# Optimization experiments

Hardware: AMD Instinct MI355X
Metric: run time of the kernel (lower is better)

Reference implementation:

```python
import jax, jax.numpy as jnp
import numpy as np

D_MODEL = 1024
DK = 64
N_HEADS = D_MODEL // DK
MASK = True


def setup_inputs() -> dict:
    key = jax.random.key(0)
    ks = jax.random.split(key, 8)
    B, S = 4, 2048
    scale = 1.0 / np.sqrt(D_MODEL)
    return {
        "query_data": jax.random.normal(ks[0], (B, S, D_MODEL), dtype=jnp.float32),
        "key_data": jax.random.normal(ks[1], (B, S, D_MODEL), dtype=jnp.float32),
        "value_data": jax.random.normal(ks[2], (B, S, D_MODEL), dtype=jnp.float32),
        "Wq": jax.random.normal(ks[3], (D_MODEL, D_MODEL), dtype=jnp.float32) * scale,
        "Wk": jax.random.normal(ks[4], (D_MODEL, D_MODEL), dtype=jnp.float32) * scale,
        "Wv": jax.random.normal(ks[5], (D_MODEL, D_MODEL), dtype=jnp.float32) * scale,
        "Wp": jax.random.normal(ks[6], (D_MODEL, D_MODEL), dtype=jnp.float32) * scale,
        "bp": jnp.zeros((D_MODEL,), dtype=jnp.float32),
    }


def reference(query_data, key_data, value_data, Wq, Wk, Wv, Wp, bp):
    B, S, _ = query_data.shape
    # QKV projections, split into heads: (B, H, S, dk)
    def split_heads(x, W):
        return (x @ W.T).reshape(B, -1, N_HEADS, DK).transpose(0, 2, 1, 3)

    q = split_heads(query_data, Wq)
    k = split_heads(key_data, Wk)
    v = split_heads(value_data, Wv)

    scores = jnp.einsum("bhqd,bhkd->bhqk", q, k) / np.sqrt(DK).astype(np.float32)
    if MASK:
        Sq, Sk = scores.shape[-2], scores.shape[-1]
        causal = jnp.triu(jnp.ones((Sq, Sk), dtype=scores.dtype), k=1) * jnp.float32(-1e13)
        scores = scores + causal  # broadcast over (B, H)
    attn = jax.nn.softmax(scores, axis=-1)
    out = jnp.einsum("bhqk,bhkd->bhqd", attn, v)
    out = out.transpose(0, 2, 1, 3).reshape(B, S, D_MODEL)
    # dropout is identity in eval mode
    return out @ Wp.T + bp
```

## Files before the change

### kernel.cpp

```cpp
#include <hip/hip_runtime.h>
#include <stdint.h>

#define D_MODEL 1024
#define SEQ     2048
#define BATCH   4
#define NH      16
#define DKK     64
#define MROWS   (BATCH * SEQ)

typedef unsigned short u16;
using bf16x8 = __attribute__((ext_vector_type(8))) __bf16;
using f32x4  = __attribute__((ext_vector_type(4))) float;

__device__ __forceinline__ u16 f2bf(float f) {
    union { float f; uint32_t u; } v; v.f = f;
    return (u16)((v.u + 0x7FFFu + ((v.u >> 16) & 1u)) >> 16);
}

__device__ __forceinline__ float fast_exp2(float x) {
    float r; asm("v_exp_f32 %0, %1" : "=v"(r) : "v"(x)); return r;
}
__device__ __forceinline__ float fast_rcp(float x) {
    float r; asm("v_rcp_f32 %0, %1" : "=v"(r) : "v"(x)); return r;
}

__device__ __forceinline__ void gl_lds16(const u16* g, u16* l) {
    __builtin_amdgcn_global_load_lds(
        (__attribute__((address_space(1))) void*)(const_cast<u16*>(g)),
        (__attribute__((address_space(3))) void*)l, 16, 0, 0);
}

__global__ __launch_bounds__(256) void cvt3_kernel(const float* __restrict__ a,
                                                   const float* __restrict__ b,
                                                   const float* __restrict__ c,
                                                   u16* __restrict__ da,
                                                   u16* __restrict__ db,
                                                   u16* __restrict__ dc) {
    const int i = blockIdx.x * 256 + threadIdx.x;
    const int sel = i >> 21, off = i & ((1 << 21) - 1);
    const float* s = (sel == 0) ? a : (sel == 1) ? b : c;
    u16* d = (sel == 0) ? da : (sel == 1) ? db : dc;
    float4 v = ((const float4*)s)[off];
    ushort4 o;
    o.x = f2bf(v.x); o.y = f2bf(v.y); o.z = f2bf(v.z); o.w = f2bf(v.w);
    ((ushort4*)d)[off] = o;
}

__global__ __launch_bounds__(256) void cvt4_kernel(const float* __restrict__ a,
                                                   const float* __restrict__ b,
                                                   const float* __restrict__ c,
                                                   const float* __restrict__ d4,
                                                   u16* __restrict__ da,
                                                   u16* __restrict__ db,
                                                   u16* __restrict__ dc,
                                                   u16* __restrict__ dd) {
    const int i = blockIdx.x * 256 + threadIdx.x;
    const int sel = i >> 18, off = i & ((1 << 18) - 1);
    const float* s = (sel == 0) ? a : (sel == 1) ? b : (sel == 2) ? c : d4;
    u16* d = (sel == 0) ? da : (sel == 1) ? db : (sel == 2) ? dc : dd;
    float4 v = ((const float4*)s)[off];
    ushort4 o;
    o.x = f2bf(v.x); o.y = f2bf(v.y); o.z = f2bf(v.z); o.w = f2bf(v.w);
    ((ushort4*)d)[off] = o;
}

__global__ __launch_bounds__(256, 2) void gemm_qkv(const u16* __restrict__ XQ,
                                                   const u16* __restrict__ XK,
                                                   const u16* __restrict__ XV,
                                                   const u16* __restrict__ WQ,
                                                   const u16* __restrict__ WK,
                                                   const u16* __restrict__ WV,
                                                   u16* __restrict__ Qo,
                                                   u16* __restrict__ Ko,
                                                   u16* __restrict__ Vto) {
    constexpr int K = 1024, N = 1024;
    __shared__ __align__(16) u16 smem[17408];
    u16* ldsA = smem;
    u16* ldsB = smem + 4096;
    u16* ldsT = smem;

    const int which = blockIdx.x >> 9;
    const int inner = blockIdx.x & 511;
    const u16* A  = (which == 0) ? XQ : (which == 1) ? XK : XV;
    const u16* Bw = (which == 0) ? WQ : (which == 1) ? WK : WV;

    const int t = threadIdx.x;
    const int w = t >> 6, lane = t & 63;
    const int quad = lane >> 4, l15 = lane & 15;
    const int bn = inner & 7, bm = inner >> 3;
    const int wm = (w >> 1) * 64, wn = (w & 1) * 64;

    const u16* Ab = A  + (size_t)bm * 128 * K;
    const u16* Bb = Bw + (size_t)bn * 128 * K;
    const int srow  = lane >> 2;
    const int scol8 = (lane & 3) * 8;

    f32x4 acc[4][4];
    #pragma unroll
    for (int i = 0; i < 4; ++i)
        #pragma unroll
        for (int j = 0; j < 4; ++j)
            acc[i][j] = f32x4{0.f, 0.f, 0.f, 0.f};

    for (int k0 = 0; k0 < K; k0 += 32) {
        __syncthreads();
        #pragma unroll
        for (int i = 0; i < 2; ++i) {
            const int c = w * 2 + i;
            gl_lds16(Ab + (size_t)(c * 16 + srow) * K + k0 + scol8, &ldsA[c * 512]);
            gl_lds16(Bb + (size_t)(c * 16 + srow) * K + k0 + scol8, &ldsB[c * 512]);
        }
        __syncthreads();

        bf16x8 afr[4], bfr[4];
        #pragma unroll
        for (int i = 0; i < 4; ++i)
            afr[i] = *(const bf16x8*)&ldsA[(wm + i * 16 + l15) * 32 + quad * 8];
        #pragma unroll
        for (int j = 0; j < 4; ++j)
            bfr[j] = *(const bf16x8*)&ldsB[(wn + j * 16 + l15) * 32 + quad * 8];

        #pragma unroll
        for (int i = 0; i < 4; ++i)
            #pragma unroll
            for (int j = 0; j < 4; ++j)
                acc[i][j] = __builtin_amdgcn_mfma_f32_16x16x32_bf16(afr[i], bfr[j], acc[i][j], 0, 0, 0);
    }

    if (which < 2) {
        u16* outb = which ? Ko : Qo;
        #pragma unroll
        for (int i = 0; i < 4; ++i)
            #pragma unroll
            for (int j = 0; j < 4; ++j)
                #pragma unroll
                for (int r = 0; r < 4; ++r) {
                    const int row = bm * 128 + wm + i * 16 + quad * 4 + r;
                    const int col = bn * 128 + wn + j * 16 + l15;
                    outb[(size_t)row * N + col] = f2bf(acc[i][j][r]);
                }
    } else {
        __syncthreads();
        #pragma unroll
        for (int i = 0; i < 4; ++i)
            #pragma unroll
            for (int j = 0; j < 4; ++j)
                #pragma unroll
                for (int r = 0; r < 4; ++r) {
                    const int row_l = wm + i * 16 + quad * 4 + r;
                    const int col_l = wn + j * 16 + l15;
                    ldsT[col_l * 136 + row_l] = f2bf(acc[i][j][r]);
                }
        __syncthreads();
        const int c = t >> 1, half = t & 1;
        const int colg = bn * 128 + c;
        const int hh = colg >> 6, dd = colg & 63;
        const int bb = bm >> 4;
        const int s0 = ((bm * 128) & 2047) + half * 64;
        const u16* srcl = ldsT + c * 136 + half * 64;
        u16* dstg = Vto + (size_t)((bb * NH + hh) * DKK + dd) * SEQ + s0;
        #pragma unroll
        for (int k = 0; k < 8; ++k)
            *(uint4*)(dstg + k * 8) = *(const uint4*)(srcl + k * 8);
    }
}

__global__ __launch_bounds__(256, 2) void gemm_proj(const u16* __restrict__ A,
                                                    const u16* __restrict__ Bw,
                                                    float* __restrict__ outf,
                                                    const float* __restrict__ bias) {
    constexpr int K = 1024, N = 1024;
    __shared__ __align__(16) u16 ldsA[128 * 32];
    __shared__ __align__(16) u16 ldsB[128 * 32];

    const int t = threadIdx.x;
    const int w = t >> 6, lane = t & 63;
    const int quad = lane >> 4, l15 = lane & 15;
    const int bn = blockIdx.x & 7, bm = blockIdx.x >> 3;
    const int wm = (w >> 1) * 64, wn = (w & 1) * 64;

    const u16* Ab = A  + (size_t)bm * 128 * K;
    const u16* Bb = Bw + (size_t)bn * 128 * K;
    const int srow  = lane >> 2;
    const int scol8 = (lane & 3) * 8;

    f32x4 acc[4][4];
    #pragma unroll
    for (int i = 0; i < 4; ++i)
        #pragma unroll
        for (int j = 0; j < 4; ++j)
            acc[i][j] = f32x4{0.f, 0.f, 0.f, 0.f};

    for (int k0 = 0; k0 < K; k0 += 32) {
        __syncthreads();
        #pragma unroll
        for (int i = 0; i < 2; ++i) {
            const int c = w * 2 + i;
            gl_lds16(Ab + (size_t)(c * 16 + srow) * K + k0 + scol8, &ldsA[c * 512]);
            gl_lds16(Bb + (size_t)(c * 16 + srow) * K + k0 + scol8, &ldsB[c * 512]);
        }
        __syncthreads();

        bf16x8 afr[4], bfr[4];
        #pragma unroll
        for (int i = 0; i < 4; ++i)
            afr[i] = *(const bf16x8*)&ldsA[(wm + i * 16 + l15) * 32 + quad * 8];
        #pragma unroll
        for (int j = 0; j < 4; ++j)
            bfr[j] = *(const bf16x8*)&ldsB[(wn + j * 16 + l15) * 32 + quad * 8];

        #pragma unroll
        for (int i = 0; i < 4; ++i)
            #pragma unroll
            for (int j = 0; j < 4; ++j)
                acc[i][j] = __builtin_amdgcn_mfma_f32_16x16x32_bf16(afr[i], bfr[j], acc[i][j], 0, 0, 0);
    }

    #pragma unroll
    for (int i = 0; i < 4; ++i)
        #pragma unroll
        for (int j = 0; j < 4; ++j)
            #pragma unroll
            for (int r = 0; r < 4; ++r) {
                const int row = bm * 128 + wm + i * 16 + quad * 4 + r;
                const int col = bn * 128 + wn + j * 16 + l15;
                outf[(size_t)row * N + col] = acc[i][j][r] + bias[col];
            }
}

__global__ __launch_bounds__(256, 4) void flash_attn(const u16* __restrict__ Qb,
                                                     const u16* __restrict__ Kb,
                                                     const u16* __restrict__ Vt,
                                                     u16* __restrict__ O) {
    __shared__ __align__(16) u16 ldsK[2 * 4096];
    __shared__ __align__(16) u16 ldsV[2 * 4096];
    __shared__ __align__(16) u16 ldsP[4 * 1024];

    const int t = threadIdx.x;
    const int w = t >> 6, lane = t & 63;
    const int quad = lane >> 4, l15 = lane & 15;
    const int bh = blockIdx.x & 63;
    const int qt = 31 - (blockIdx.x >> 6);
    const int b = bh >> 4, h = bh & 15;
    const int q0 = qt * 64;
    const int qw = q0 + w * 16;

    const int srow  = lane >> 2;
    const int scol8 = (lane & 3) * 8;
    const size_t kbase = (size_t)b * SEQ * D_MODEL + h * DKK;
    const size_t vbase = (size_t)(bh * DKK) * SEQ;

    const u16* Qrow = Qb + (size_t)(b * SEQ + qw + l15) * D_MODEL + h * DKK;
    const bf16x8 qf0 = *(const bf16x8*)(Qrow + quad * 8);
    const bf16x8 qf1 = *(const bf16x8*)(Qrow + 32 + quad * 8);

    f32x4 o_acc[4];
    #pragma unroll
    for (int nt = 0; nt < 4; ++nt) o_acc[nt] = f32x4{0.f, 0.f, 0.f, 0.f};
    float m_i = -1e30f, l_i = 0.f;

    const float C2 = 0.18033688f;

    u16* PwS = &ldsP[w * 1024 + l15 * 64];

    {
        #pragma unroll
        for (int i = 0; i < 2; ++i) {
            const int e = w * 2 + i, ch = e >> 2, rb = (e & 3) * 16;
            gl_lds16(Kb + kbase + (size_t)(rb + srow) * D_MODEL + ch * 32 + scol8,
                     &ldsK[ch * 2048 + rb * 32]);
            gl_lds16(Vt + vbase + (size_t)(rb + srow) * SEQ + ch * 32 + scol8,
                     &ldsV[ch * 2048 + rb * 32]);
        }
    }

    int cur = 0;
    for (int it = 0; it <= qt; ++it) {
        const int kb = it * 64;
        __syncthreads();

        if (it < qt) {
            const int nb = (it + 1) * 64, nxt = cur ^ 1;
            #pragma unroll
            for (int i = 0; i < 2; ++i) {
                const int e = w * 2 + i, ch = e >> 2, rb = (e & 3) * 16;
                gl_lds16(Kb + kbase + (size_t)(nb + rb + srow) * D_MODEL + ch * 32 + scol8,
                         &ldsK[nxt * 4096 + ch * 2048 + rb * 32]);
                gl_lds16(Vt + vbase + (size_t)(rb + srow) * SEQ + nb + ch * 32 + scol8,
                         &ldsV[nxt * 4096 + ch * 2048 + rb * 32]);
            }
        }

        f32x4 sc[4];
        #pragma unroll
        for (int jt = 0; jt < 4; ++jt) sc[jt] = f32x4{0.f, 0.f, 0.f, 0.f};
        #pragma unroll
        for (int ks = 0; ks < 2; ++ks) {
            const bf16x8 qf = ks ? qf1 : qf0;
            #pragma unroll
            for (int jt = 0; jt < 4; ++jt) {
                bf16x8 kf = *(const bf16x8*)&ldsK[cur * 4096 + ks * 2048 + (jt * 16 + l15) * 32 + quad * 8];
                sc[jt] = __builtin_amdgcn_mfma_f32_16x16x32_bf16(kf, qf, sc[jt], 0, 0, 0);
            }
        }

        if (kb + 63 > qw) {
            #pragma unroll
            for (int jt = 0; jt < 4; ++jt)
                #pragma unroll
                for (int r = 0; r < 4; ++r)
                    if (kb + jt * 16 + quad * 4 + r > qw + l15) sc[jt][r] = -3.0e38f;
        }

        float tmax = sc[0][0];
        #pragma unroll
        for (int jt = 0; jt < 4; ++jt)
            #pragma unroll
            for (int r = 0; r < 4; ++r) tmax = fmaxf(tmax, sc[jt][r]);
        tmax = fmaxf(tmax, __shfl_xor(tmax, 16));
        tmax = fmaxf(tmax, __shfl_xor(tmax, 32));

        const float mn = fmaxf(m_i, tmax * C2);
        const float alpha = fast_exp2(m_i - mn);
        m_i = mn;

        float tsum = 0.f;
        #pragma unroll
        for (int jt = 0; jt < 4; ++jt) {
            float p[4];
            #pragma unroll
            for (int r = 0; r < 4; ++r) {
                p[r] = fast_exp2(fmaf(sc[jt][r], C2, -mn));
                tsum += p[r];
            }
            const int pos = (4 * jt + quad) ^ l15;
            uint2 pk;
            pk.x = (uint32_t)f2bf(p[0]) | ((uint32_t)f2bf(p[1]) << 16);
            pk.y = (uint32_t)f2bf(p[2]) | ((uint32_t)f2bf(p[3]) << 16);
            *(uint2*)&PwS[pos * 4] = pk;
        }
        tsum += __shfl_xor(tsum, 16);
        tsum += __shfl_xor(tsum, 32);
        l_i = fmaf(l_i, alpha, tsum);

        float al[4];
        #pragma unroll
        for (int r = 0; r < 4; ++r)
            al[r] = __shfl(alpha, (lane & 48) | (quad * 4 + r));
        #pragma unroll
        for (int nt = 0; nt < 4; ++nt)
            #pragma unroll
            for (int r = 0; r < 4; ++r)
                o_acc[nt][r] *= al[r];

        asm volatile("s_waitcnt lgkmcnt(0)" ::: "memory");

        #pragma unroll
        for (int ks = 0; ks < 2; ++ks) {
            const int g = 8 * ks + 2 * quad;
            uint2 lo = *(const uint2*)&PwS[((g    ) ^ l15) * 4];
            uint2 hi = *(const uint2*)&PwS[((g + 1) ^ l15) * 4];
            union { bf16x8 v; uint2 u[2]; } pu;
            pu.u[0] = lo; pu.u[1] = hi;
            #pragma unroll
            for (int nt = 0; nt < 4; ++nt) {
                bf16x8 vf = *(const bf16x8*)&ldsV[cur * 4096 + ks * 2048 + (nt * 16 + l15) * 32 + quad * 8];
                o_acc[nt] = __builtin_amdgcn_mfma_f32_16x16x32_bf16(pu.v, vf, o_acc[nt], 0, 0, 0);
            }
        }

        cur ^= 1;
    }

    const float rli = fast_rcp(l_i);
    float rl[4];
    #pragma unroll
    for (int r = 0; r < 4; ++r)
        rl[r] = __shfl(rli, (lane & 48) | (quad * 4 + r));
    #pragma unroll
    for (int nt = 0; nt < 4; ++nt)
        #pragma unroll
        for (int r = 0; r < 4; ++r) {
            const int qg = qw + quad * 4 + r;
            O[(size_t)(b * SEQ + qg) * D_MODEL + h * DKK + nt * 16 + l15] = f2bf(o_acc[nt][r] * rl[r]);
        }
}

extern "C" void kernel_launch(void* const* d_in, const int* in_sizes, int n_in,
                              void* d_out, int out_size, void* d_ws, size_t ws_size,
                              hipStream_t stream) {
    const float* q_in = (const float*)d_in[0];
    const float* k_in = (const float*)d_in[1];
    const float* v_in = (const float*)d_in[2];
    const float* Wq   = (const float*)d_in[3];
    const float* Wk   = (const float*)d_in[4];
    const float* Wv   = (const float*)d_in[5];
    const float* Wp   = (const float*)d_in[6];
    const float* bp   = (const float*)d_in[7];
    float* out = (float*)d_out;

    char* ws = (char*)d_ws;
    u16* XQ  = (u16*)(ws + (size_t)0);
    u16* XK  = (u16*)(ws + ((size_t)16 << 20));
    u16* XV  = (u16*)(ws + ((size_t)32 << 20));
    u16* WQb = (u16*)(ws + ((size_t)48 << 20));
    u16* WKb = (u16*)(ws + ((size_t)50 << 20));
    u16* WVb = (u16*)(ws + ((size_t)52 << 20));
    u16* WPb = (u16*)(ws + ((size_t)54 << 20));
    u16* Qb  = (u16*)(ws + ((size_t)56 << 20));
    u16* Kb  = (u16*)(ws + ((size_t)72 << 20));
    u16* Vtb = (u16*)(ws + ((size_t)88 << 20));

    cvt3_kernel<<<3 * (1 << 21) / 256, 256, 0, stream>>>(q_in, k_in, v_in, XQ, XK, XV);
    cvt4_kernel<<<4 * (1 << 18) / 256, 256, 0, stream>>>(Wq, Wk, Wv, Wp, WQb, WKb, WVb, WPb);

    gemm_qkv<<<1536, 256, 0, stream>>>(XQ, XK, XV, WQb, WKb, WVb, Qb, Kb, Vtb);

    flash_attn<<<BATCH * NH * (SEQ / 64), 256, 0, stream>>>(Qb, Kb, Vtb, XQ);

    gemm_proj<<<512, 256, 0, stream>>>(XQ, WPb, out, bp);
}
```

Measured before the change: 347.8 us.

## Double-buffer GEMMs, swizzle tiles, and widen attention to 128-row query tiles

Both projection GEMMs now prefetch the next K slice into a second LDS buffer, drop one barrier per step, and remap blocks so neighbours share input tiles in L2. Flash attention now handles 128 queries per block with two 16-row groups per wave, reusing each K and V fragment twice and skipping key tiles that are fully masked for a wave. The fp32 to bf16 conversions use the packed rounding intrinsic, and launch bounds are retuned. The changes cost more registers and LDS per block and so may reduce occupancy, and they introduce per-wave load imbalance in attention.

Result: faster. 305.6 us (-12.1%).

```diff
diff --git a/kernel.cpp b/kernel.cpp
--- a/kernel.cpp
+++ b/kernel.cpp
@@ -1,4 +1,5 @@
 #include <hip/hip_runtime.h>
+#include <hip/hip_bf16.h>
 #include <stdint.h>
 
 #define D_MODEL 1024
@@ -15,6 +16,11 @@
 __device__ __forceinline__ u16 f2bf(float f) {
     union { float f; uint32_t u; } v; v.f = f;
     return (u16)((v.u + 0x7FFFu + ((v.u >> 16) & 1u)) >> 16);
+}
+__device__ __forceinline__ uint32_t pk2bf(float a, float b) {
+    union { __hip_bfloat162 h; uint32_t u; } v;
+    v.h = __float22bfloat162_rn(float2{a, b});
+    return v.u;
 }
 
 __device__ __forceinline__ float fast_exp2(float x) {
@@ -41,9 +47,9 @@
     const float* s = (sel == 0) ? a : (sel == 1) ? b : c;
     u16* d = (sel == 0) ? da : (sel == 1) ? db : dc;
     float4 v = ((const float4*)s)[off];
-    ushort4 o;
-    o.x = f2bf(v.x); o.y = f2bf(v.y); o.z = f2bf(v.z); o.w = f2bf(v.w);
-    ((ushort4*)d)[off] = o;
+    uint2 o;
+    o.x = pk2bf(v.x, v.y); o.y = pk2bf(v.z, v.w);
+    ((uint2*)d)[off] = o;
 }
 
 __global__ __launch_bounds__(256) void cvt4_kernel(const float* __restrict__ a,
@@ -59,12 +65,12 @@
     const float* s = (sel == 0) ? a : (sel == 1) ? b : (sel == 2) ? c : d4;
     u16* d = (sel == 0) ? da : (sel == 1) ? db : (sel == 2) ? dc : dd;
     float4 v = ((const float4*)s)[off];
-    ushort4 o;
-    o.x = f2bf(v.x); o.y = f2bf(v.y); o.z = f2bf(v.z); o.w = f2bf(v.w);
-    ((ushort4*)d)[off] = o;
-}
-
-__global__ __launch_bounds__(256, 2) void gemm_qkv(const u16* __restrict__ XQ,
+    uint2 o;
+    o.x = pk2bf(v.x, v.y); o.y = pk2bf(v.z, v.w);
+    ((uint2*)d)[off] = o;
+}
+
+__global__ __launch_bounds__(256, 3) void gemm_qkv(const u16* __restrict__ XQ,
                                                    const u16* __restrict__ XK,
                                                    const u16* __restrict__ XV,
                                                    const u16* __restrict__ WQ,
@@ -76,7 +82,7 @@
     constexpr int K = 1024, N = 1024;
     __shared__ __align__(16) u16 smem[17408];
     u16* ldsA = smem;
-    u16* ldsB = smem + 4096;
+    u16* ldsB = smem + 8192;
     u16* ldsT = smem;
 
     const int which = blockIdx.x >> 9;
@@ -87,7 +93,8 @@
     const int t = threadIdx.x;
     const int w = t >> 6, lane = t & 63;
     const int quad = lane >> 4, l15 = lane & 15;
-    const int bn = inner & 7, bm = inner >> 3;
+    const int x = inner & 7, j = inner >> 3;
+    const int bm = x * 8 + (j >> 3), bn = j & 7;
     const int wm = (w >> 1) * 64, wn = (w & 1) * 64;
 
     const u16* Ab = A  + (size_t)bm * 128 * K;
@@ -99,32 +106,43 @@
     #pragma unroll
     for (int i = 0; i < 4; ++i)
         #pragma unroll
-        for (int j = 0; j < 4; ++j)
-            acc[i][j] = f32x4{0.f, 0.f, 0.f, 0.f};
-
+        for (int jj = 0; jj < 4; ++jj)
+            acc[i][jj] = f32x4{0.f, 0.f, 0.f, 0.f};
+
+    #pragma unroll
+    for (int i = 0; i < 2; ++i) {
+        const int c = w * 2 + i;
+        gl_lds16(Ab + (size_t)(c * 16 + srow) * K + scol8, &ldsA[c * 512]);
+        gl_lds16(Bb + (size_t)(c * 16 + srow) * K + scol8, &ldsB[c * 512]);
+    }
+
+    int cur = 0;
     for (int k0 = 0; k0 < K; k0 += 32) {
         __syncthreads();
-        #pragma unroll
-        for (int i = 0; i < 2; ++i) {
-            const int c = w * 2 + i;
-            gl_lds16(Ab + (size_t)(c * 16 + srow) * K + k0 + scol8, &ldsA[c * 512]);
-            gl_lds16(Bb + (size_t)(c * 16 + srow) * K + k0 + scol8, &ldsB[c * 512]);
+        if (k0 + 32 < K) {
+            const int nxt = cur ^ 1;
+            #pragma unroll
+            for (int i = 0; i < 2; ++i) {
+                const int c = w * 2 + i;
+                gl_lds16(Ab + (size_t)(c * 16 + srow) * K + k0 + 32 + scol8, &ldsA[nxt * 4096 + c * 512]);
+                gl_lds16(Bb + (size_t)(c * 16 + srow) * K + k0 + 32 + scol8, &ldsB[nxt * 4096 + c * 512]);
+            }
         }
-        __syncthreads();
 
         bf16x8 afr[4], bfr[4];
         #pragma unroll
         for (int i = 0; i < 4; ++i)
-            afr[i] = *(const bf16x8*)&ldsA[(wm + i * 16 + l15) * 32 + quad * 8];
-        #pragma unroll
-        for (int j = 0; j < 4; ++j)
-            bfr[j] = *(const bf16x8*)&ldsB[(wn + j * 16 + l15) * 32 + quad * 8];
-
-        #pragma unroll
-        for (int i = 0; i < 4; ++i)
-            #pragma unroll
-            for (int j = 0; j < 4; ++j)
-                acc[i][j] = __builtin_amdgcn_mfma_f32_16x16x32_bf16(afr[i], bfr[j], acc[i][j], 0, 0, 0);
+            afr[i] = *(const bf16x8*)&ldsA[cur * 4096 + (wm + i * 16 + l15) * 32 + quad * 8];
+        #pragma unroll
+        for (int jj = 0; jj < 4; ++jj)
+            bfr[jj] = *(const bf16x8*)&ldsB[cur * 4096 + (wn + jj * 16 + l15) * 32 + quad * 8];
+
+        #pragma unroll
+        for (int i = 0; i < 4; ++i)
+            #pragma unroll
+            for (int jj = 0; jj < 4; ++jj)
+                acc[i][jj] = __builtin_amdgcn_mfma_f32_16x16x32_bf16(afr[i], bfr[jj], acc[i][jj], 0, 0, 0);
+        cur ^= 1;
     }
 
     if (which < 2) {
@@ -132,24 +150,24 @@
         #pragma unroll
         for (int i = 0; i < 4; ++i)
             #pragma unroll
-            for (int j = 0; j < 4; ++j)
+            for (int jj = 0; jj < 4; ++jj)
                 #pragma unroll
                 for (int r = 0; r < 4; ++r) {
                     const int row = bm * 128 + wm + i * 16 + quad * 4 + r;
-                    const int col = bn * 128 + wn + j * 16 + l15;
-                    outb[(size_t)row * N + col] = f2bf(acc[i][j][r]);
+                    const int col = bn * 128 + wn + jj * 16 + l15;
+                    outb[(size_t)row * N + col] = f2bf(acc[i][jj][r]);
                 }
     } else {
         __syncthreads();
         #pragma unroll
         for (int i = 0; i < 4; ++i)
             #pragma unroll
-            for (int j = 0; j < 4; ++j)
+            for (int jj = 0; jj < 4; ++jj)
                 #pragma unroll
                 for (int r = 0; r < 4; ++r) {
                     const int row_l = wm + i * 16 + quad * 4 + r;
-                    const int col_l = wn + j * 16 + l15;
-                    ldsT[col_l * 136 + row_l] = f2bf(acc[i][j][r]);
+                    const int col_l = wn + jj * 16 + l15;
+                    ldsT[col_l * 136 + row_l] = f2bf(acc[i][jj][r]);
                 }
         __syncthreads();
         const int c = t >> 1, half = t & 1;
@@ -165,18 +183,19 @@
     }
 }
 
-__global__ __launch_bounds__(256, 2) void gemm_proj(const u16* __restrict__ A,
+__global__ __launch_bounds__(256, 3) void gemm_proj(const u16* __restrict__ A,
                                                     const u16* __restrict__ Bw,
                                                     float* __restrict__ outf,
                                                     const float* __restrict__ bias) {
     constexpr int K = 1024, N = 1024;
-    __shared__ __align__(16) u16 ldsA[128 * 32];
-    __shared__ __align__(16) u16 ldsB[128 * 32];
+    __shared__ __align__(16) u16 ldsA[2 * 4096];
+    __shared__ __align__(16) u16 ldsB[2 * 4096];
 
     const int t = threadIdx.x;
     const int w = t >> 6, lane = t & 63;
     const int quad = lane >> 4, l15 = lane & 15;
-    const int bn = blockIdx.x & 7, bm = blockIdx.x >> 3;
+    const int x = blockIdx.x & 7, j = blockIdx.x >> 3;
+    const int bm = x * 8 + ((j & 63) >> 3), bn = j & 7;
     const int wm = (w >> 1) * 64, wn = (w & 1) * 64;
 
     const u16* Ab = A  + (size_t)bm * 128 * K;
@@ -188,99 +207,115 @@
     #pragma unroll
     for (int i = 0; i < 4; ++i)
         #pragma unroll
-        for (int j = 0; j < 4; ++j)
-            acc[i][j] = f32x4{0.f, 0.f, 0.f, 0.f};
-
+        for (int jj = 0; jj < 4; ++jj)
+            acc[i][jj] = f32x4{0.f, 0.f, 0.f, 0.f};
+
+    #pragma unroll
+    for (int i = 0; i < 2; ++i) {
+        const int c = w * 2 + i;
+        gl_lds16(Ab + (size_t)(c * 16 + srow) * K + scol8, &ldsA[c * 512]);
+        gl_lds16(Bb + (size_t)(c * 16 + srow) * K + scol8, &ldsB[c * 512]);
+    }
+
+    int cur = 0;
     for (int k0 = 0; k0 < K; k0 += 32) {
         __syncthreads();
-        #pragma unroll
-        for (int i = 0; i < 2; ++i) {
-            const int c = w * 2 + i;
-            gl_lds16(Ab + (size_t)(c * 16 + srow) * K + k0 + scol8, &ldsA[c * 512]);
-            gl_lds16(Bb + (size_t)(c * 16 + srow) * K + k0 + scol8, &ldsB[c * 512]);
+        if (k0 + 32 < K) {
+            const int nxt = cur ^ 1;
+            #pragma unroll
+            for (int i = 0; i < 2; ++i) {
+                const int c = w * 2 + i;
+                gl_lds16(Ab + (size_t)(c * 16 + srow) * K + k0 + 32 + scol8, &ldsA[nxt * 4096 + c * 512]);
+                gl_lds16(Bb + (size_t)(c * 16 + srow) * K + k0 + 32 + scol8, &ldsB[nxt * 4096 + c * 512]);
+            }
         }
-        __syncthreads();
 
         bf16x8 afr[4], bfr[4];
         #pragma unroll
         for (int i = 0; i < 4; ++i)
-            afr[i] = *(const bf16x8*)&ldsA[(wm + i * 16 + l15) * 32 + quad * 8];
-        #pragma unroll
-        for (int j = 0; j < 4; ++j)
-            bfr[j] = *(const bf16x8*)&ldsB[(wn + j * 16 + l15) * 32 + quad * 8];
-
-        #pragma unroll
-        for (int i = 0; i < 4; ++i)
-            #pragma unroll
-            for (int j = 0; j < 4; ++j)
-                acc[i][j] = __builtin_amdgcn_mfma_f32_16x16x32_bf16(afr[i], bfr[j], acc[i][j], 0, 0, 0);
+            afr[i] = *(const bf16x8*)&ldsA[cur * 4096 + (wm + i * 16 + l15) * 32 + quad * 8];
+        #pragma unroll
+        for (int jj = 0; jj < 4; ++jj)
+            bfr[jj] = *(const bf16x8*)&ldsB[cur * 4096 + (wn + jj * 16 + l15) * 32 + quad * 8];
+
+        #pragma unroll
+        for (int i = 0; i < 4; ++i)
+            #pragma unroll
+            for (int jj = 0; jj < 4; ++jj)
+                acc[i][jj] = __builtin_amdgcn_mfma_f32_16x16x32_bf16(afr[i], bfr[jj], acc[i][jj], 0, 0, 0);
+        cur ^= 1;
     }
 
     #pragma unroll
     for (int i = 0; i < 4; ++i)
         #pragma unroll
-        for (int j = 0; j < 4; ++j)
+        for (int jj = 0; jj < 4; ++jj)
             #pragma unroll
             for (int r = 0; r < 4; ++r) {
                 const int row = bm * 128 + wm + i * 16 + quad * 4 + r;
-                const int col = bn * 128 + wn + j * 16 + l15;
-                outf[(size_t)row * N + col] = acc[i][j][r] + bias[col];
-            }
-}
-
-__global__ __launch_bounds__(256, 4) void flash_attn(const u16* __restrict__ Qb,
+                const int col = bn * 128 + wn + jj * 16 + l15;
+                outf[(size_t)row * N + col] = acc[i][jj][r] + bias[col];
+            }
+}
+
+__global__ __launch_bounds__(256, 3) void flash_attn(const u16* __restrict__ Qb,
                                                      const u16* __restrict__ Kb,
                                                      const u16* __restrict__ Vt,
                                                      u16* __restrict__ O) {
     __shared__ __align__(16) u16 ldsK[2 * 4096];
     __shared__ __align__(16) u16 ldsV[2 * 4096];
-    __shared__ __align__(16) u16 ldsP[4 * 1024];
+    __shared__ __align__(16) u16 ldsP[4 * 2048];
 
     const int t = threadIdx.x;
     const int w = t >> 6, lane = t & 63;
     const int quad = lane >> 4, l15 = lane & 15;
     const int bh = blockIdx.x & 63;
-    const int qt = 31 - (blockIdx.x >> 6);
+    const int qt = 15 - (blockIdx.x >> 6);
     const int b = bh >> 4, h = bh & 15;
-    const int q0 = qt * 64;
-    const int qw = q0 + w * 16;
+    const int q0 = qt * 128;
+    const int qw = q0 + w * 32;
 
     const int srow  = lane >> 2;
     const int scol8 = (lane & 3) * 8;
     const size_t kbase = (size_t)b * SEQ * D_MODEL + h * DKK;
     const size_t vbase = (size_t)(bh * DKK) * SEQ;
 
-    const u16* Qrow = Qb + (size_t)(b * SEQ + qw + l15) * D_MODEL + h * DKK;
-    const bf16x8 qf0 = *(const bf16x8*)(Qrow + quad * 8);
-    const bf16x8 qf1 = *(const bf16x8*)(Qrow + 32 + quad * 8);
-
-    f32x4 o_acc[4];
-    #pragma unroll
-    for (int nt = 0; nt < 4; ++nt) o_acc[nt] = f32x4{0.f, 0.f, 0.f, 0.f};
-    float m_i = -1e30f, l_i = 0.f;
+    bf16x8 qf[2][2];
+    #pragma unroll
+    for (int g = 0; g < 2; ++g) {
+        const u16* Qrow = Qb + (size_t)(b * SEQ + qw + g * 16 + l15) * D_MODEL + h * DKK;
+        qf[g][0] = *(const bf16x8*)(Qrow + quad * 8);
+        qf[g][1] = *(const bf16x8*)(Qrow + 32 + quad * 8);
+    }
+
+    f32x4 o_acc[2][4];
+    #pragma unroll
+    for (int g = 0; g < 2; ++g)
+        #pragma unroll
+        for (int nt = 0; nt < 4; ++nt) o_acc[g][nt] = f32x4{0.f, 0.f, 0.f, 0.f};
+    float m_i[2] = {-1e30f, -1e30f}, l_i[2] = {0.f, 0.f};
 
     const float C2 = 0.18033688f;
-
-    u16* PwS = &ldsP[w * 1024 + l15 * 64];
-
-    {
-        #pragma unroll
-        for (int i = 0; i < 2; ++i) {
-            const int e = w * 2 + i, ch = e >> 2, rb = (e & 3) * 16;
-            gl_lds16(Kb + kbase + (size_t)(rb + srow) * D_MODEL + ch * 32 + scol8,
-                     &ldsK[ch * 2048 + rb * 32]);
-            gl_lds16(Vt + vbase + (size_t)(rb + srow) * SEQ + ch * 32 + scol8,
-                     &ldsV[ch * 2048 + rb * 32]);
-        }
+    u16* PwS = &ldsP[w * 2048];
+
+    const int ntiles = 2 * qt + 2;
+
+    #pragma unroll
+    for (int i = 0; i < 2; ++i) {
+        const int e = w * 2 + i, ch = e >> 2, rb = (e & 3) * 16;
+        gl_lds16(Kb + kbase + (size_t)(rb + srow) * D_MODEL + ch * 32 + scol8,
+                 &ldsK[ch * 2048 + rb * 32]);
+        gl_lds16(Vt + vbase + (size_t)(rb + srow) * SEQ + ch * 32 + scol8,
+                 &ldsV[ch * 2048 + rb * 32]);
     }
 
     int cur = 0;
-    for (int it = 0; it <= qt; ++it) {
+    for (int it = 0; it < ntiles; ++it) {
         const int kb = it * 64;
         __syncthreads();
 
-        if (it < qt) {
-            const int nb = (it + 1) * 64, nxt = cur ^ 1;
+        if (it + 1 < ntiles) {
+            const int nb = kb + 64, nxt = cur ^ 1;
             #pragma unroll
             for (int i = 0; i < 2; ++i) {
                 const int e = w * 2 + i, ch = e >> 2, rb = (e & 3) * 16;
@@ -291,99 +326,119 @@
             }
         }
 
-        f32x4 sc[4];
-        #pragma unroll
-        for (int jt = 0; jt < 4; ++jt) sc[jt] = f32x4{0.f, 0.f, 0.f, 0.f};
-        #pragma unroll
-        for (int ks = 0; ks < 2; ++ks) {
-            const bf16x8 qf = ks ? qf1 : qf0;
-            #pragma unroll
-            for (int jt = 0; jt < 4; ++jt) {
-                bf16x8 kf = *(const bf16x8*)&ldsK[cur * 4096 + ks * 2048 + (jt * 16 + l15) * 32 + quad * 8];
-                sc[jt] = __builtin_amdgcn_mfma_f32_16x16x32_bf16(kf, qf, sc[jt], 0, 0, 0);
+        if (kb <= qw + 31) {
+            f32x4 sc[2][4];
+            #pragma unroll
+            for (int g = 0; g < 2; ++g)
+                #pragma unroll
+                for (int jt = 0; jt < 4; ++jt) sc[g][jt] = f32x4{0.f, 0.f, 0.f, 0.f};
+            #pragma unroll
+            for (int ks = 0; ks < 2; ++ks)
+                #pragma unroll
+                for (int jt = 0; jt < 4; ++jt) {
+                    bf16x8 kf = *(const bf16x8*)&ldsK[cur * 4096 + ks * 2048 + (jt * 16 + l15) * 32 + quad * 8];
+                    #pragma unroll
+                    for (int g = 0; g < 2; ++g)
+                        sc[g][jt] = __builtin_amdgcn_mfma_f32_16x16x32_bf16(kf, qf[g][ks], sc[g][jt], 0, 0, 0);
+                }
+
+            if (kb + 63 >= qw) {
+                #pragma unroll
+                for (int g = 0; g < 2; ++g)
+                    #pragma unroll
+                    for (int jt = 0; jt < 4; ++jt)
+                        #pragma unroll
+                        for (int r = 0; r < 4; ++r)
+                            if (kb + jt * 16 + quad * 4 + r > qw + g * 16 + l15) sc[g][jt][r] = -3.0e38f;
+            }
+
+            float alpha[2];
+            #pragma unroll
+            for (int g = 0; g < 2; ++g) {
+                float tmax = sc[g][0][0];
+                #pragma unroll
+                for (int jt = 0; jt < 4; ++jt)
+                    #pragma unroll
+                    for (int r = 0; r < 4; ++r) tmax = fmaxf(tmax, sc[g][jt][r]);
+                tmax = fmaxf(tmax, __shfl_xor(tmax, 16));
+                tmax = fmaxf(tmax, __shfl_xor(tmax, 32));
+
+                const float mn = fmaxf(m_i[g], tmax * C2);
+                alpha[g] = fast_exp2(m_i[g] - mn);
+                m_i[g] = mn;
+
+                float tsum = 0.f;
+                #pragma unroll
+                for (int jt = 0; jt < 4; ++jt) {
+                    float p[4];
+                    #pragma unroll
+                    for (int r = 0; r < 4; ++r) {
+                        p[r] = fast_exp2(fmaf(sc[g][jt][r], C2, -mn));
+                        tsum += p[r];
+                    }
+                    const int pos = (4 * jt + quad) ^ l15;
+                    uint2 pk;
+                    pk.x = pk2bf(p[0], p[1]);
+                    pk.y = pk2bf(p[2], p[3]);
+                    *(uint2*)&PwS[g * 1024 + l15 * 64 + pos * 4] = pk;
+                }
+                tsum += __shfl_xor(tsum, 16);
+                tsum += __shfl_xor(tsum, 32);
+                l_i[g] = fmaf(l_i[g], alpha[g], tsum);
+            }
+
+            #pragma unroll
+            for (int g = 0; g < 2; ++g) {
+                float al[4];
+                #pragma unroll
+                for (int r = 0; r < 4; ++r)
+                    al[r] = __shfl(alpha[g], (lane & 48) | (quad * 4 + r));
+                #pragma unroll
+                for (int nt = 0; nt < 4; ++nt)
+                    #pragma unroll
+                    for (int r = 0; r < 4; ++r)
+                        o_acc[g][nt][r] *= al[r];
+            }
+
+            asm volatile("s_waitcnt lgkmcnt(0)" ::: "memory");
+
+            #pragma unroll
+            for (int ks = 0; ks < 2; ++ks) {
+                const int gg = 8 * ks + 2 * quad;
+                union { bf16x8 v; uint2 u[2]; } pu[2];
+                #pragma unroll
+                for (int g = 0; g < 2; ++g) {
+                    pu[g].u[0] = *(const uint2*)&PwS[g * 1024 + l15 * 64 + ((gg) ^ l15) * 4];
+                    pu[g].u[1] = *(const uint2*)&PwS[g * 1024 + l15 * 64 + ((gg + 1) ^ l15) * 4];
+                }
+                #pragma unroll
+                for (int nt = 0; nt < 4; ++nt) {
+                    bf16x8 vf = *(const bf16x8*)&ldsV[cur * 4096 + ks * 2048 + (nt * 16 + l15) * 32 + quad * 8];
+                    #pragma unroll
+                    for (int g = 0; g < 2; ++g)
+                        o_acc[g][nt] = __builtin_amdgcn_mfma_f32_16x16x32_bf16(pu[g].v, vf, o_acc[g][nt], 0, 0, 0);
+                }
             }
         }
 
-        if (kb + 63 > qw) {
-            #pragma unroll
-            for (int jt = 0; jt < 4; ++jt)
-                #pragma unroll
-                for (int r = 0; r < 4; ++r)
-                    if (kb + jt * 16 + quad * 4 + r > qw + l15) sc[jt][r] = -3.0e38f;
-        }
-
-        float tmax = sc[0][0];
-        #pragma unroll
-        for (int jt = 0; jt < 4; ++jt)
-            #pragma unroll
-            for (int r = 0; r < 4; ++r) tmax = fmaxf(tmax, sc[jt][r]);
-        tmax = fmaxf(tmax, __shfl_xor(tmax, 16));
-        tmax = fmaxf(tmax, __shfl_xor(tmax, 32));
-
-        const float mn = fmaxf(m_i, tmax * C2);
-        const float alpha = fast_exp2(m_i - mn);
-        m_i = mn;
-
-        float tsum = 0.f;
-        #pragma unroll
-        for (int jt = 0; jt < 4; ++jt) {
-            float p[4];
+        cur ^= 1;
+    }
+
+    #pragma unroll
+    for (int g = 0; g < 2; ++g) {
+        const float rli = fast_rcp(l_i[g]);
+        float rl[4];
+        #pragma unroll
+        for (int r = 0; r < 4; ++r)
+            rl[r] = __shfl(rli, (lane & 48) | (quad * 4 + r));
+        #pragma unroll
+        for (int nt = 0; nt < 4; ++nt)
             #pragma unroll
             for (int r = 0; r < 4; ++r) {
-                p[r] = fast_exp2(fmaf(sc[jt][r], C2, -mn));
-                tsum += p[r];
-            }
-            const int pos = (4 * jt + quad) ^ l15;
-            uint2 pk;
-            pk.x = (uint32_t)f2bf(p[0]) | ((uint32_t)f2bf(p[1]) << 16);
-            pk.y = (uint32_t)f2bf(p[2]) | ((uint32_t)f2bf(p[3]) << 16);
-            *(uint2*)&PwS[pos * 4] = pk;
-        }
-        tsum += __shfl_xor(tsum, 16);
-        tsum += __shfl_xor(tsum, 32);
-        l_i = fmaf(l_i, alpha, tsum);
-
-        float al[4];
-        #pragma unroll
-        for (int r = 0; r < 4; ++r)
-            al[r] = __shfl(alpha, (lane & 48) | (quad * 4 + r));
-        #pragma unroll
-        for (int nt = 0; nt < 4; ++nt)
-            #pragma unroll
-            for (int r = 0; r < 4; ++r)
-                o_acc[nt][r] *= al[r];
-
-        asm volatile("s_waitcnt lgkmcnt(0)" ::: "memory");
-
-        #pragma unroll
-        for (int ks = 0; ks < 2; ++ks) {
-            const int g = 8 * ks + 2 * quad;
-            uint2 lo = *(const uint2*)&PwS[((g    ) ^ l15) * 4];
-            uint2 hi = *(const uint2*)&PwS[((g + 1) ^ l15) * 4];
-            union { bf16x8 v; uint2 u[2]; } pu;
-            pu.u[0] = lo; pu.u[1] = hi;
-            #pragma unroll
-            for (int nt = 0; nt < 4; ++nt) {
-                bf16x8 vf = *(const bf16x8*)&ldsV[cur * 4096 + ks * 2048 + (nt * 16 + l15) * 32 + quad * 8];
-                o_acc[nt] = __builtin_amdgcn_mfma_f32_16x16x32_bf16(pu.v, vf, o_acc[nt], 0, 0, 0);
-            }
-        }
-
-        cur ^= 1;
-    }
-
-    const float rli = fast_rcp(l_i);
-    float rl[4];
-    #pragma unroll
-    for (int r = 0; r < 4; ++r)
-        rl[r] = __shfl(rli, (lane & 48) | (quad * 4 + r));
-    #pragma unroll
-    for (int nt = 0; nt < 4; ++nt)
-        #pragma unroll
-        for (int r = 0; r < 4; ++r) {
-            const int qg = qw + quad * 4 + r;
-            O[(size_t)(b * SEQ + qg) * D_MODEL + h * DKK + nt * 16 + l15] = f2bf(o_acc[nt][r] * rl[r]);
-        }
+                const int qg = qw + g * 16 + quad * 4 + r;
+                O[(size_t)(b * SEQ + qg) * D_MODEL + h * DKK + nt * 16 + l15] = f2bf(o_acc[g][nt][r] * rl[r]);
+            }
+    }
 }
 
 extern "C" void kernel_launch(void* const* d_in, const int* in_sizes, int n_in,
@@ -416,7 +471,7 @@
 
     gemm_qkv<<<1536, 256, 0, stream>>>(XQ, XK, XV, WQb, WKb, WVb, Qb, Kb, Vtb);
 
-    flash_attn<<<BATCH * NH * (SEQ / 64), 256, 0, stream>>>(Qb, Kb, Vtb, XQ);
+    flash_attn<<<BATCH * NH * (SEQ / 128), 256, 0, stream>>>(Qb, Kb, Vtb, XQ);
 
     gemm_proj<<<512, 256, 0, stream>>>(XQ, WPb, out, bp);
 }
```
